# Kernel tuning notes

Hardware: AMD Instinct MI355X
Metric: run time of the kernel (lower is better)

The kernel has to match this reference:

```python
import jax, jax.numpy as jnp
import numpy as np

B, V, F = 32, 1024, 16
A, P, NF = 32, 64, 128
C = P + A  # propagated feature width after concat with edge weights
D_OUT_IN = F + A + 2 * A * C  # 6192, input dim of output Dense


def setup_inputs() -> dict:
    key = jax.random.key(0)
    ks = jax.random.split(key, 4)
    return {
        "x": jax.random.normal(ks[0], (B, V, F), dtype=jnp.float32),
        "W_flr": jax.random.normal(ks[1], (F, P), dtype=jnp.float32) * (1.0 / np.sqrt(F)),
        "b_flr": jnp.zeros((P,), dtype=jnp.float32),
        "W_s": jax.random.normal(ks[2], (F, A), dtype=jnp.float32) * (1.0 / np.sqrt(F)),
        "b_s": jnp.zeros((A,), dtype=jnp.float32),
        "W_out": jax.random.normal(ks[3], (D_OUT_IN, NF), dtype=jnp.float32) * (1.0 / np.sqrt(D_OUT_IN)),
        "b_out": jnp.zeros((NF,), dtype=jnp.float32),
    }


def reference(x, W_flr, b_flr, W_s, b_s, W_out, b_out):
    # Per-vertex transforms
    feat = x @ W_flr + b_flr                      # (B,V,P)
    dist = x @ W_s + b_s                          # (B,V,A)
    ew = jnp.exp(-jnp.square(dist))               # (B,V,A) edge weights vertex->aggregator
    f = jnp.concatenate([feat, ew], axis=-1)      # (B,V,C)

    # Weighted broadcast then vertex-axis reduction (aggregator gather)
    w = jnp.transpose(ew, (0, 2, 1))              # (B,A,V)
    prod = w[..., None] * f[:, None, :, :]        # (B,A,V,C)
    agg_max = jnp.max(prod, axis=2)               # (B,A,C)
    agg_mean = jnp.mean(prod, axis=2)             # (B,A,C)
    agg = jnp.concatenate([agg_max, agg_mean], axis=-1)  # (B,A,2C)

    # Scatter aggregated features back to vertices, weighted by same edge weights
    upd = ew[..., None] * agg[:, None, :, :]      # (B,V,A,2C)
    upd = upd.reshape(B, V, A * 2 * C)            # (B,V,2AC)

    cat = jnp.concatenate([x, upd, ew], axis=-1)  # (B,V,F+2AC+A)
    return jnp.tanh(cat @ W_out + b_out)          # (B,V,NF)
```

## Files before the change

kernel.cpp:

```cpp
#include <hip/hip_runtime.h>
#include <hip/hip_bf16.h>
#include <math.h>

#define NB 32
#define NV 1024
#define NFT 16
#define NA 32
#define NP 64
#define NOUT 128
#define NC 96
#define NC2 192

#define NSPLIT 16
#define VPB 64

typedef __attribute__((ext_vector_type(8))) short bf16x8;
typedef __attribute__((ext_vector_type(4))) float f32x4;

__global__ void k2p(const float* __restrict__ x,
                    const float* __restrict__ W_flr,
                    const float* __restrict__ b_flr,
                    const float* __restrict__ W_s,
                    const float* __restrict__ b_s,
                    float* __restrict__ ewbuf,
                    float* __restrict__ part) {
    __shared__ float xs[VPB][NFT];
    __shared__ float fs[VPB][NC];
    __shared__ float pcomb[(31 * 100 + 95) * 2 + 2];

    int b = blockIdx.x, vs = blockIdx.y, tid = threadIdx.x;
    int rowbase = b * NV + vs * VPB;

    {
        const float4* xsrc = (const float4*)(x + (size_t)rowbase * NFT);
        ((float4*)xs)[tid] = xsrc[tid];
    }
    __syncthreads();

    {
        int c  = tid & 127;
        int rh = tid >> 7;
        if (c < NC) {
            float Wcol[NFT], bias;
            if (c < NP) {
                bias = b_flr[c];
#pragma unroll
                for (int k = 0; k < NFT; ++k) Wcol[k] = W_flr[k * NP + c];
            } else {
                int a = c - NP;
                bias = b_s[a];
#pragma unroll
                for (int k = 0; k < NFT; ++k) Wcol[k] = W_s[k * NA + a];
            }
#pragma unroll
            for (int r0 = 0; r0 < 32; ++r0) {
                int r = rh * 32 + r0;
                float xr[NFT];
#pragma unroll
                for (int q = 0; q < 4; ++q)
                    ((float4*)xr)[q] = ((const float4*)xs[r])[q];
                float acc = bias;
#pragma unroll
                for (int k = 0; k < NFT; ++k)
                    acc = fmaf(xr[k], Wcol[k], acc);
                if (c >= NP) {
                    acc = __expf(-acc * acc);
                    ewbuf[(size_t)(rowbase + r) * NA + (c - NP)] = acc;
                }
                fs[r][c] = acc;
            }
        }
    }
    __syncthreads();

    int grp = tid >> 7;
    int gl  = tid & 127;
    int at = gl >> 4, ct = gl & 15;
    int a0 = at * 4, c0 = ct * 6;
    int rbase = grp * 32;

    float sm[4][6], mx[4][6];
#pragma unroll
    for (int i = 0; i < 4; ++i)
#pragma unroll
        for (int j = 0; j < 6; ++j) { sm[i][j] = 0.f; mx[i][j] = -INFINITY; }

#pragma unroll 4
    for (int r0 = 0; r0 < 32; ++r0) {
        int r = rbase + r0;
        float4 e4 = *(const float4*)&fs[r][NP + a0];
        float2 fA = *(const float2*)&fs[r][c0];
        float2 fB = *(const float2*)&fs[r][c0 + 2];
        float2 fC = *(const float2*)&fs[r][c0 + 4];
        float ff[6] = {fA.x, fA.y, fB.x, fB.y, fC.x, fC.y};
        float ee[4] = {e4.x, e4.y, e4.z, e4.w};
#pragma unroll
        for (int i = 0; i < 4; ++i)
#pragma unroll
            for (int j = 0; j < 6; ++j) {
                float p = ee[i] * ff[j];
                sm[i][j] += p;
                mx[i][j] = fmaxf(mx[i][j], p);
            }
    }

    if (grp == 0) {
#pragma unroll
        for (int i = 0; i < 4; ++i) {
            int base = ((a0 + i) * 100 + c0) * 2;
#pragma unroll
            for (int q = 0; q < 3; ++q) {
                float4 v = {sm[i][2 * q], mx[i][2 * q], sm[i][2 * q + 1], mx[i][2 * q + 1]};
                *(float4*)&pcomb[base + q * 4] = v;
            }
        }
    }
    __syncthreads();
    if (grp == 1) {
        float* pb = part + (size_t)((b * NSPLIT + vs) * NA) * NC2;
#pragma unroll
        for (int i = 0; i < 4; ++i) {
            int base = ((a0 + i) * 100 + c0) * 2;
            float osm[6], omx[6];
#pragma unroll
            for (int q = 0; q < 3; ++q) {
                float4 v = *(const float4*)&pcomb[base + q * 4];
                osm[2 * q] = v.x; omx[2 * q] = v.y;
                osm[2 * q + 1] = v.z; omx[2 * q + 1] = v.w;
            }
            int a = a0 + i;
#pragma unroll
            for (int q = 0; q < 3; ++q) {
                float2 vm = {fmaxf(mx[i][2 * q], omx[2 * q]),
                             fmaxf(mx[i][2 * q + 1], omx[2 * q + 1])};
                float2 vsum = {sm[i][2 * q] + osm[2 * q],
                               sm[i][2 * q + 1] + osm[2 * q + 1]};
                *(float2*)&pb[a * NC2 + c0 + 2 * q]      = vm;
                *(float2*)&pb[a * NC2 + NC + c0 + 2 * q] = vsum;
            }
        }
    }
}

__global__ void k23(const float* __restrict__ part,
                    const float* __restrict__ W_out,
                    float* __restrict__ Gp) {
    __shared__ float aggL[NC2];
    int b = blockIdx.x, a = blockIdx.y, tid = threadIdx.x;

    {
        const float* pb = part + (size_t)(b * NSPLIT * NA + a) * NC2 + tid;
        const size_t stride = (size_t)NA * NC2;
        if (tid < NC) {
            float m = -INFINITY;
#pragma unroll
            for (int vsi = 0; vsi < NSPLIT; ++vsi)
                m = fmaxf(m, pb[vsi * stride]);
            aggL[tid] = m;
        } else {
            float s = 0.f;
#pragma unroll
            for (int vsi = 0; vsi < NSPLIT; ++vsi)
                s += pb[vsi * stride];
            aggL[tid] = s * (1.0f / (float)NV);
        }
    }
    __syncthreads();

    if (tid < NOUT) {
        int n = tid;
        const float* wr = W_out + (size_t)(NFT + a * NC2) * NOUT + n;
        float acc = W_out[(size_t)(NFT + NA * NC2 + a) * NOUT + n];
#pragma unroll 8
        for (int c = 0; c < NC2; ++c)
            acc = fmaf(aggL[c], wr[(size_t)c * NOUT], acc);
        Gp[(size_t)(b * NA + a) * NOUT + n] = acc;
    }
}

#define MB 64
#define SWZ(r, k)  (((r) << 6) + ((k) ^ (((r) & 7) << 3)))
#define SWZB(n, k) (((n) << 6) + ((k) ^ (((((n) >> 3) & 7) ^ ((n) & 7)) << 3)))

__device__ inline void f2hl(float v, ushort& h, ushort& l) {
    __hip_bfloat16 hb = __float2bfloat16(v);
    float hf = __bfloat162float(hb);
    __hip_bfloat16 lb = __float2bfloat16(v - hf);
    h = *(ushort*)&hb;
    l = *(ushort*)&lb;
}

__global__ void k4_mfma(const float* __restrict__ x,
                        const float* __restrict__ ewbuf,
                        const float* __restrict__ Gp,
                        const float* __restrict__ W_out,
                        const float* __restrict__ b_out,
                        float* __restrict__ out) {
    __shared__ ushort AsH[MB * 64], AsL[MB * 64];
    __shared__ ushort BsH[NOUT * 64], BsL[NOUT * 64];
    __shared__ float  bs[NOUT];

    int rb = blockIdx.x;
    int b  = blockIdx.y;
    int tid = threadIdx.x;
    int rowbase = b * NV + rb * MB;

    {
        float4 v = ((const float4*)(x + (size_t)rowbase * NFT))[tid];
        int r = tid >> 2, kq = (tid & 3) * 4;
        float vv[4] = {v.x, v.y, v.z, v.w};
        ushort h[4], l[4];
#pragma unroll
        for (int j = 0; j < 4; ++j) f2hl(vv[j], h[j], l[j]);
        *(uint*)&AsH[SWZ(r, kq)]     = (uint)h[0] | ((uint)h[1] << 16);
        *(uint*)&AsH[SWZ(r, kq + 2)] = (uint)h[2] | ((uint)h[3] << 16);
        *(uint*)&AsL[SWZ(r, kq)]     = (uint)l[0] | ((uint)l[1] << 16);
        *(uint*)&AsL[SWZ(r, kq + 2)] = (uint)l[2] | ((uint)l[3] << 16);
    }
    {
        const float4* es4 = (const float4*)(ewbuf + (size_t)rowbase * NA);
#pragma unroll
        for (int t = 0; t < 2; ++t) {
            int i = tid * 2 + t;
            float4 v = es4[i];
            int r = i >> 3, kq = 16 + (i & 7) * 4;
            float vv[4] = {v.x, v.y, v.z, v.w};
            ushort h[4], l[4];
#pragma unroll
            for (int j = 0; j < 4; ++j) f2hl(vv[j], h[j], l[j]);
            *(uint*)&AsH[SWZ(r, kq)]     = (uint)h[0] | ((uint)h[1] << 16);
            *(uint*)&AsH[SWZ(r, kq + 2)] = (uint)h[2] | ((uint)h[3] << 16);
            *(uint*)&AsL[SWZ(r, kq)]     = (uint)l[0] | ((uint)l[1] << 16);
            *(uint*)&AsL[SWZ(r, kq + 2)] = (uint)l[2] | ((uint)l[3] << 16);
        }
    }
    {
#pragma unroll
        for (int t = 0; t < 2; ++t) {
            int i = tid * 2 + t;
            int r = i >> 3, kq = 48 + (i & 7) * 2;
            *(uint*)&AsH[SWZ(r, kq)] = 0u;
            *(uint*)&AsL[SWZ(r, kq)] = 0u;
        }
    }
    {
#pragma unroll
        for (int t = 0; t < 2; ++t) {
            int i = tid * 2 + t;
            int k = i >> 5, nq = (i & 31) * 4;
            float4 v = ((const float4*)W_out)[i];
            float vv[4] = {v.x, v.y, v.z, v.w};
#pragma unroll
            for (int j = 0; j < 4; ++j) {
                ushort h, l;
                f2hl(vv[j], h, l);
                BsH[SWZB(nq + j, k)] = h;
                BsL[SWZB(nq + j, k)] = l;
            }
        }
    }
    {
        const float4* gp4 = (const float4*)(Gp + (size_t)b * NA * NOUT);
#pragma unroll
        for (int t = 0; t < 4; ++t) {
            int i = tid * 4 + t;
            int a = i >> 5, nq = (i & 31) * 4;
            float4 v = gp4[i];
            int k = 16 + a;
            float vv[4] = {v.x, v.y, v.z, v.w};
#pragma unroll
            for (int j = 0; j < 4; ++j) {
                ushort h, l;
                f2hl(vv[j], h, l);
                BsH[SWZB(nq + j, k)] = h;
                BsL[SWZB(nq + j, k)] = l;
            }
        }
    }
    {
#pragma unroll
        for (int t = 0; t < 4; ++t) {
            int i = tid * 4 + t;
            int n = i >> 3, kq = 48 + (i & 7) * 2;
            *(uint*)&BsH[SWZB(n, kq)] = 0u;
            *(uint*)&BsL[SWZB(n, kq)] = 0u;
        }
    }
    if (tid < NOUT) bs[tid] = b_out[tid];

    __syncthreads();

    int w = tid >> 6, lane = tid & 63;
    int r16 = lane & 15, kg = lane >> 4, k0 = kg * 8;
    int arow = w * 16 + r16;

    bf16x8 AH0 = *(const bf16x8*)&AsH[SWZ(arow, k0)];
    bf16x8 AH1 = *(const bf16x8*)&AsH[SWZ(arow, 32 + k0)];
    bf16x8 AL0 = *(const bf16x8*)&AsL[SWZ(arow, k0)];
    bf16x8 AL1 = *(const bf16x8*)&AsL[SWZ(arow, 32 + k0)];

    int orow0 = rowbase + w * 16 + kg * 4;

#pragma unroll
    for (int nt = 0; nt < 8; ++nt) {
        int n = nt * 16 + r16;
        bf16x8 BH0 = *(const bf16x8*)&BsH[SWZB(n, k0)];
        bf16x8 BH1 = *(const bf16x8*)&BsH[SWZB(n, 32 + k0)];
        bf16x8 BL0 = *(const bf16x8*)&BsL[SWZB(n, k0)];
        bf16x8 BL1 = *(const bf16x8*)&BsL[SWZB(n, 32 + k0)];
        float bias = bs[n];
        f32x4 acc = {bias, bias, bias, bias};
        acc = __builtin_amdgcn_mfma_f32_16x16x32_bf16(AH0, BH0, acc, 0, 0, 0);
        acc = __builtin_amdgcn_mfma_f32_16x16x32_bf16(AL0, BH0, acc, 0, 0, 0);
        acc = __builtin_amdgcn_mfma_f32_16x16x32_bf16(AH0, BL0, acc, 0, 0, 0);
        acc = __builtin_amdgcn_mfma_f32_16x16x32_bf16(AH1, BH1, acc, 0, 0, 0);
        acc = __builtin_amdgcn_mfma_f32_16x16x32_bf16(AL1, BH1, acc, 0, 0, 0);
        acc = __builtin_amdgcn_mfma_f32_16x16x32_bf16(AH1, BL1, acc, 0, 0, 0);
#pragma unroll
        for (int rg = 0; rg < 4; ++rg) {
            float s = acc[rg];
            s = fminf(fmaxf(s, -15.f), 15.f);
            float e = __expf(2.f * s);
            out[(size_t)(orow0 + rg) * NOUT + n] =
                (e - 1.f) * __builtin_amdgcn_rcpf(e + 1.f);
        }
    }
}

extern "C" void kernel_launch(void* const* d_in, const int* in_sizes, int n_in,
                              void* d_out, int out_size, void* d_ws, size_t ws_size,
                              hipStream_t stream) {
    const float* x     = (const float*)d_in[0];
    const float* W_flr = (const float*)d_in[1];
    const float* b_flr = (const float*)d_in[2];
    const float* W_s   = (const float*)d_in[3];
    const float* b_s   = (const float*)d_in[4];
    const float* W_out = (const float*)d_in[5];
    const float* b_out = (const float*)d_in[6];
    float* out = (float*)d_out;

    float* ewbuf = (float*)d_ws;
    float* part  = ewbuf + (size_t)NB * NV * NA;
    float* Gp    = part  + (size_t)NB * NSPLIT * NA * NC2;

    {
        dim3 g(NB, NSPLIT);
        k2p<<<g, 256, 0, stream>>>(x, W_flr, b_flr, W_s, b_s, ewbuf, part);
    }
    {
        dim3 g(NB, NA);
        k23<<<g, 192, 0, stream>>>(part, W_out, Gp);
    }
    {
        dim3 g(NV / MB, NB);
        k4_mfma<<<g, 256, 0, stream>>>(x, ewbuf, Gp, W_out, b_out, out);
    }
}
```

Before: 38.58 us.

## Widen k2p to 512 threads with one aggregator per thread, drop LDS combine

```diff
diff --git a/kernel.cpp b/kernel.cpp
--- a/kernel.cpp
+++ b/kernel.cpp
@@ -17,21 +17,21 @@
 typedef __attribute__((ext_vector_type(8))) short bf16x8;
 typedef __attribute__((ext_vector_type(4))) float f32x4;
 
-__global__ void k2p(const float* __restrict__ x,
-                    const float* __restrict__ W_flr,
-                    const float* __restrict__ b_flr,
-                    const float* __restrict__ W_s,
-                    const float* __restrict__ b_s,
-                    float* __restrict__ ewbuf,
-                    float* __restrict__ part) {
+__global__ __launch_bounds__(512, 2)
+void k2p(const float* __restrict__ x,
+         const float* __restrict__ W_flr,
+         const float* __restrict__ b_flr,
+         const float* __restrict__ W_s,
+         const float* __restrict__ b_s,
+         float* __restrict__ ewbuf,
+         float* __restrict__ part) {
     __shared__ float xs[VPB][NFT];
     __shared__ float fs[VPB][NC];
-    __shared__ float pcomb[(31 * 100 + 95) * 2 + 2];
 
     int b = blockIdx.x, vs = blockIdx.y, tid = threadIdx.x;
     int rowbase = b * NV + vs * VPB;
 
-    {
+    if (tid < 256) {
         const float4* xsrc = (const float4*)(x + (size_t)rowbase * NFT);
         ((float4*)xs)[tid] = xsrc[tid];
     }
@@ -53,8 +53,8 @@
                 for (int k = 0; k < NFT; ++k) Wcol[k] = W_s[k * NA + a];
             }
 #pragma unroll
-            for (int r0 = 0; r0 < 32; ++r0) {
-                int r = rh * 32 + r0;
+            for (int r0 = 0; r0 < 16; ++r0) {
+                int r = rh * 16 + r0;
                 float xr[NFT];
 #pragma unroll
                 for (int q = 0; q < 4; ++q)
@@ -73,72 +73,36 @@
     }
     __syncthreads();
 
-    int grp = tid >> 7;
-    int gl  = tid & 127;
-    int at = gl >> 4, ct = gl & 15;
-    int a0 = at * 4, c0 = ct * 6;
-    int rbase = grp * 32;
-
-    float sm[4][6], mx[4][6];
-#pragma unroll
-    for (int i = 0; i < 4; ++i)
-#pragma unroll
-        for (int j = 0; j < 6; ++j) { sm[i][j] = 0.f; mx[i][j] = -INFINITY; }
+    int a  = tid >> 4;
+    int c0 = (tid & 15) * 6;
+    int ea = NP + a;
+
+    float sm[6], mx[6];
+#pragma unroll
+    for (int j = 0; j < 6; ++j) { sm[j] = 0.f; mx[j] = -INFINITY; }
 
 #pragma unroll 4
-    for (int r0 = 0; r0 < 32; ++r0) {
-        int r = rbase + r0;
-        float4 e4 = *(const float4*)&fs[r][NP + a0];
+    for (int r = 0; r < VPB; ++r) {
+        float e = fs[r][ea];
         float2 fA = *(const float2*)&fs[r][c0];
         float2 fB = *(const float2*)&fs[r][c0 + 2];
         float2 fC = *(const float2*)&fs[r][c0 + 4];
         float ff[6] = {fA.x, fA.y, fB.x, fB.y, fC.x, fC.y};
-        float ee[4] = {e4.x, e4.y, e4.z, e4.w};
-#pragma unroll
-        for (int i = 0; i < 4; ++i)
-#pragma unroll
-            for (int j = 0; j < 6; ++j) {
-                float p = ee[i] * ff[j];
-                sm[i][j] += p;
-                mx[i][j] = fmaxf(mx[i][j], p);
-            }
-    }
-
-    if (grp == 0) {
-#pragma unroll
-        for (int i = 0; i < 4; ++i) {
-            int base = ((a0 + i) * 100 + c0) * 2;
-#pragma unroll
-            for (int q = 0; q < 3; ++q) {
-                float4 v = {sm[i][2 * q], mx[i][2 * q], sm[i][2 * q + 1], mx[i][2 * q + 1]};
-                *(float4*)&pcomb[base + q * 4] = v;
-            }
-        }
-    }
-    __syncthreads();
-    if (grp == 1) {
-        float* pb = part + (size_t)((b * NSPLIT + vs) * NA) * NC2;
-#pragma unroll
-        for (int i = 0; i < 4; ++i) {
-            int base = ((a0 + i) * 100 + c0) * 2;
-            float osm[6], omx[6];
-#pragma unroll
-            for (int q = 0; q < 3; ++q) {
-                float4 v = *(const float4*)&pcomb[base + q * 4];
-                osm[2 * q] = v.x; omx[2 * q] = v.y;
-                osm[2 * q + 1] = v.z; omx[2 * q + 1] = v.w;
-            }
-            int a = a0 + i;
-#pragma unroll
-            for (int q = 0; q < 3; ++q) {
-                float2 vm = {fmaxf(mx[i][2 * q], omx[2 * q]),
-                             fmaxf(mx[i][2 * q + 1], omx[2 * q + 1])};
-                float2 vsum = {sm[i][2 * q] + osm[2 * q],
-                               sm[i][2 * q + 1] + osm[2 * q + 1]};
-                *(float2*)&pb[a * NC2 + c0 + 2 * q]      = vm;
-                *(float2*)&pb[a * NC2 + NC + c0 + 2 * q] = vsum;
-            }
-        }
+#pragma unroll
+        for (int j = 0; j < 6; ++j) {
+            float p = e * ff[j];
+            sm[j] += p;
+            mx[j] = fmaxf(mx[j], p);
+        }
+    }
+
+    float* pb = part + (size_t)((b * NSPLIT + vs) * NA + a) * NC2;
+#pragma unroll
+    for (int q = 0; q < 3; ++q) {
+        float2 vm = {mx[2 * q], mx[2 * q + 1]};
+        float2 vsum = {sm[2 * q], sm[2 * q + 1]};
+        *(float2*)&pb[c0 + 2 * q]      = vm;
+        *(float2*)&pb[NC + c0 + 2 * q] = vsum;
     }
 }
 
@@ -345,7 +309,7 @@
 
     {
         dim3 g(NB, NSPLIT);
-        k2p<<<g, 256, 0, stream>>>(x, W_flr, b_flr, W_s, b_s, ewbuf, part);
+        k2p<<<g, 512, 0, stream>>>(x, W_flr, b_flr, W_s, b_s, ewbuf, part);
     }
     {
         dim3 g(NB, NA);
```

Measured after the change: 38.07 us. About the same (-1.3%).
